# Optimization experiments

Measured on AMD Instinct MI355X. Metric: run time of the kernel, lower is better.

The kernel has to match this reference:

```python
import math
import jax, jax.numpy as jnp
import numpy as np

N = 10000      # num_nodes
E = 320000     # num_edges (avg degree 32)
D = 256        # hidden_dim
H = 8          # num_heads
HD = D // H    # head_dim = 32
S = 3          # num_scales
SCALES = (1.0, 2.0, 4.0)
BASE_MD = 500.0   # max_distance
RADIUS = 50.0     # spatial density radius


def setup_inputs() -> dict:
    key = jax.random.key(0)
    ks = jax.random.split(key, 24)
    nrm = lambda k, shape, s=0.02: jax.random.normal(k, shape, jnp.float32) * s
    return {
        "x": jax.random.normal(ks[0], (N, D), jnp.float32),
        "coords": jax.random.uniform(ks[1], (N, 2), jnp.float32) * 1000.0,
        "edge_index": jax.random.randint(ks[2], (2, E), 0, N, jnp.int32),
        "Wq": nrm(ks[3], (S, D, D)),
        "Wk": nrm(ks[4], (S, D, D)),
        "Wv": nrm(ks[5], (S, D, D)),
        "Wo": nrm(ks[6], (S, D, D)),
        "bo": jnp.zeros((S, D), jnp.float32),
        "temp": jnp.ones((S, H), jnp.float32),
        "dist_emb": nrm(ks[7], (S, 100, HD // 2)),
        "dir_emb": nrm(ks[8], (S, 16, HD // 2)),
        "Wsp1": nrm(ks[9], (S, HD, HD)),
        "bsp1": jnp.zeros((S, HD), jnp.float32),
        "Wsp2": nrm(ks[10], (S, 1, HD)),
        "bsp2": jnp.zeros((S, 1), jnp.float32),
        "Wd1": nrm(ks[11], (S, D // 2, 3)),
        "bd1": jnp.zeros((S, D // 2), jnp.float32),
        "Wd2": nrm(ks[12], (S, D, D // 2)),
        "bd2": jnp.zeros((S, D), jnp.float32),
        "Wf": nrm(ks[13], (D, S * D)),
        "bf": jnp.zeros((D,), jnp.float32),
    }


def reference(x, coords, edge_index, Wq, Wk, Wv, Wo, bo, temp, dist_emb, dir_emb,
              Wsp1, bsp1, Wsp2, bsp2, Wd1, bd1, Wd2, bd2, Wf, bf):
    src, dst = edge_index[0], edge_index[1]   # row=source j, col/dst=target i
    n = x.shape[0]
    eps = 1e-8

    # ---- shared density statistics (same math in every scale's encoder) ----
    ones_e = jnp.ones(src.shape[0], jnp.float32)
    deg = jax.ops.segment_sum(ones_e, src, num_segments=n)
    deg_n = deg / (deg.max() + eps)
    # spatial density: count of neighbors within RADIUS via full cdist (as in torch)
    c = jax.lax.stop_gradient(coords)  # only used via thresholds / integer bins -> zero grad
    d2 = jnp.sqrt(jnp.maximum(((c[:, None, :] - c[None, :, :]) ** 2).sum(-1), 0.0))
    sp = (d2 <= RADIUS).sum(axis=1).astype(jnp.float32) - 1.0
    sp = sp / (sp.max() + eps)
    # local feature variance
    nbr_sum = jax.ops.segment_sum(x[dst], src, num_segments=n)
    cnt = jnp.maximum(deg, 1.0)[:, None]
    fvar = jnp.linalg.norm(x - nbr_sum / cnt, axis=-1)
    fvar = fvar / (fvar.max() + eps)
    dens_raw = jnp.stack([deg_n, sp, fvar], axis=-1)  # [N, 3]

    # ---- shared relative geometry (binned -> no grad through coords) ----
    rel = c[src] - c[dst]                       # coords_j - coords_i
    dist = jnp.linalg.norm(rel, axis=-1)        # [E]
    ang = jnp.arctan2(rel[:, 1], rel[:, 0])
    abin = jnp.clip(((ang + math.pi) / (2.0 * math.pi) * 15.0).astype(jnp.int32), 0, 15)

    outs = []
    for s in range(S):
        md = BASE_MD * SCALES[s]
        dbin = jnp.clip((dist / md * 99.0).astype(jnp.int32), 0, 99)
        se = jnp.concatenate([dist_emb[s][dbin], dir_emb[s][abin]], axis=-1)  # [E, HD]
        enc = (jax.nn.relu(se @ Wsp1[s].T + bsp1[s]) @ Wsp2[s].T + bsp2[s])[:, 0]  # [E]

        df = jax.nn.relu(dens_raw @ Wd1[s].T + bd1[s]) @ Wd2[s].T + bd2[s]  # [N, D]

        q = (x @ Wq[s].T).reshape(n, H, HD)
        k = (x @ Wk[s].T).reshape(n, H, HD)
        v = (x @ Wv[s].T).reshape(n, H, HD)

        scores = (q[dst] * k[src]).sum(-1) / math.sqrt(HD)  # [E, H]
        scores = scores / temp[s][None, :]
        scores = scores + enc[:, None]
        dfi, dfj = df[dst], df[src]
        dsim = (dfi * dfj).sum(-1) / (jnp.maximum(jnp.linalg.norm(dfi, axis=-1), eps)
                                       * jnp.maximum(jnp.linalg.norm(dfj, axis=-1), eps))
        scores = scores * (1.0 + 0.5 * dsim[:, None])

        # scatter-softmax over edges grouped by destination node
        smax = jax.ops.segment_max(scores, dst, num_segments=n)
        p = jnp.exp(scores - smax[dst])
        z = jax.ops.segment_sum(p, dst, num_segments=n)
        probs = p / (z[dst] + 1e-16)

        agg = jax.ops.segment_sum(probs[..., None] * v[src], dst, num_segments=n)
        outs.append(agg.reshape(n, D) @ Wo[s].T + bo[s])

    fused = jnp.concatenate(outs, axis=-1) @ Wf.T + bf
    return fused
```

## Files before the change

### kernel.cpp

```cpp
#include <hip/hip_runtime.h>

typedef _Float16 f16;
typedef _Float16 f16x4 __attribute__((ext_vector_type(4)));
typedef _Float16 f16x8 __attribute__((ext_vector_type(8)));
typedef float    f32x4 __attribute__((ext_vector_type(4)));
typedef float    fv2   __attribute__((ext_vector_type(2)));

__device__ __forceinline__ float4 ld4h(const f16* p) {
  f16x4 t = *(const f16x4*)p;
  return make_float4((float)t[0], (float)t[1], (float)t[2], (float)t[3]);
}

__device__ __forceinline__ float4 dec_fp8x4(unsigned u) {
  fv2 lo = __builtin_amdgcn_cvt_pk_f32_fp8(u, false);
  fv2 hi = __builtin_amdgcn_cvt_pk_f32_fp8(u, true);
  return make_float4(lo[0], lo[1], hi[0], hi[1]);
}

__device__ __forceinline__ unsigned enc_fp8x4(float a, float b, float c, float d) {
  unsigned v = 0;
  v = __builtin_amdgcn_cvt_pk_fp8_f32(a, b, v, false);
  v = __builtin_amdgcn_cvt_pk_fp8_f32(c, d, v, true);
  return v;
}

__device__ __forceinline__ void gld_lds16(const void* g, void* l) {
  __builtin_amdgcn_global_load_lds(
      (const __attribute__((address_space(1))) unsigned*)g,
      (__attribute__((address_space(3))) unsigned*)l, 16, 0, 0);
}

__device__ __forceinline__ int cell_of(const float* coords, int i) {
  int cx = (int)(coords[2 * i] * 0.02f);
  int cy = (int)(coords[2 * i + 1] * 0.02f);
  cx = cx < 0 ? 0 : (cx > 19 ? 19 : cx);
  cy = cy < 0 ? 0 : (cy > 19 ? 19 : cy);
  return cy * 20 + cx;
}

__device__ __forceinline__ void gemm_core(
    f16* As, f16* Bs, int bx, int by, int s,
    const f16* __restrict__ A, int lda, long sA,
    const f16* __restrict__ B, int ldb, long sB,
    const float* __restrict__ bias, int sBias,
    void* __restrict__ Cv, int ldc, long sC, int K, int Mstore, int outMode,
    unsigned char* __restrict__ Cv2, int ldc2, long sC2, int ysplit)
{
  const int tid = threadIdx.x;
  const int lane = tid & 63;
  const int w = tid >> 6;
  const int wr = (w >> 1) * 64, wc = (w & 1) * 64;
  const int srow = tid >> 3;
  const int scol = (((tid & 7) ^ (srow & 7))) * 8;
  const f16* Ab = A + (size_t)s * sA + (size_t)(bx * 128 + srow) * lda + scol;
  const f16* Bb = B + (size_t)s * sB + (size_t)(by * 128 + srow) * ldb + scol;
  char* Asl = (char*)As + tid * 16;
  char* Bsl = (char*)Bs + tid * 16;

  f32x4 acc[4][4] = {};

  for (int kt = 0; kt < K; kt += 64) {
    __syncthreads();
#pragma unroll
    for (int i = 0; i < 4; ++i) {
      gld_lds16(Ab + (size_t)i * 32 * lda + kt, Asl + i * 4096);
      gld_lds16(Bb + (size_t)i * 32 * ldb + kt, Bsl + i * 4096);
    }
    __syncthreads();
#pragma unroll
    for (int kq = 0; kq < 2; ++kq) {
      const int krd = kq * 32 + (lane >> 4) * 8;
      const int kc = krd >> 3;
      f16x8 af[4], bfr[4];
#pragma unroll
      for (int t = 0; t < 4; ++t) {
        const int ra = wr + t * 16 + (lane & 15);
        const int rb = wc + t * 16 + (lane & 15);
        af[t]  = *(const f16x8*)&As[ra * 64 + (kc ^ (ra & 7)) * 8];
        bfr[t] = *(const f16x8*)&Bs[rb * 64 + (kc ^ (rb & 7)) * 8];
      }
#pragma unroll
      for (int mi = 0; mi < 4; ++mi)
#pragma unroll
        for (int ni = 0; ni < 4; ++ni)
          acc[mi][ni] = __builtin_amdgcn_mfma_f32_16x16x32_f16(af[mi], bfr[ni], acc[mi][ni], 0, 0, 0);
    }
  }

  const int r0 = (lane >> 4) << 2;
  const int c0 = lane & 15;
  const bool f8p = (by >= ysplit);
  const int cbase = f8p ? (by - ysplit) * 128 : by * 128;
#pragma unroll
  for (int mi = 0; mi < 4; ++mi) {
#pragma unroll
    for (int ni = 0; ni < 4; ++ni) {
      int col = cbase + wc + ni * 16 + c0;
      float bv = (!f8p && bias) ? bias[s * sBias + col] : 0.0f;
#pragma unroll
      for (int r = 0; r < 4; ++r) {
        int row = bx * 128 + wr + mi * 16 + r0 + r;
        if (row < Mstore) {
          float v = acc[mi][ni][r] + bv;
          if (f8p) {
            unsigned pk = __builtin_amdgcn_cvt_pk_fp8_f32(v, v, 0u, false);
            Cv2[(size_t)s * sC2 + (size_t)row * ldc2 + col] = (unsigned char)(pk & 0xffu);
          } else if (outMode == 1) {
            ((f16*)Cv)[(size_t)s * sC + (size_t)row * ldc + col] = (f16)v;
          } else {
            ((float*)Cv)[(size_t)s * sC + (size_t)row * ldc + col] = v;
          }
        }
      }
    }
  }
}

__global__ __launch_bounds__(256) void prep_kernel(
    const float* __restrict__ x, const float* __restrict__ Wq, const float* __restrict__ Wk,
    const float* __restrict__ Wv, const float* __restrict__ Wd2,
    f16* __restrict__ x_h, unsigned* __restrict__ x8, f16* __restrict__ wqvk,
    f16* __restrict__ wd2h,
    const float* __restrict__ dist_emb, const float* __restrict__ dir_emb,
    const float* __restrict__ Wsp1, const float* __restrict__ bsp1,
    const float* __restrict__ Wsp2, const float* __restrict__ bsp2,
    float* __restrict__ enc_tab,
    const int* __restrict__ eidx, const float* __restrict__ coords,
    int* deg_i, int* indeg_i, int* cellcnt,
    const float* __restrict__ Wf, const float* __restrict__ Wo,
    const float* __restrict__ bo, const float* __restrict__ bf,
    f16* __restrict__ wfo, float* __restrict__ bias_f,
    int E, int N, int hb)
{
  const int b = blockIdx.x;
  if (b < 2048) {
    const int n0 = N * 64;
    const int total = n0 + 147456 + 24576;
    for (int i = b * 256 + threadIdx.x; i < total; i += 2048 * 256) {
      int k = i;
      if (k < n0) {
        float4 v = ((const float4*)x)[k];
        f16x4 o; o[0] = (f16)v.x; o[1] = (f16)v.y; o[2] = (f16)v.z; o[3] = (f16)v.w;
        ((f16x4*)x_h)[k] = o;
        x8[k] = enc_fp8x4(v.x, v.y, v.z, v.w);
        continue;
      }
      const float4* sp; f16x4* dp;
      k -= n0;
      if (k < 147456) {
        int s = k / 49152, r = k % 49152, m = r / 16384, off = r % 16384;
        const float* w = (m == 0) ? Wq : (m == 1) ? Wk : Wv;
        int dblk = (m == 0) ? 0 : (m == 1) ? 32768 : 16384;
        sp = (const float4*)(w + s * 65536) + off;
        dp = (f16x4*)wqvk + s * 49152 + dblk + off;
      } else {
        k -= 147456;
        sp = (const float4*)Wd2 + k; dp = (f16x4*)wd2h + k;
      }
      float4 v = *sp;
      f16x4 o; o[0] = (f16)v.x; o[1] = (f16)v.y; o[2] = (f16)v.z; o[3] = (f16)v.w;
      *dp = o;
    }
  } else if (b < 2067) {
    int id = (b - 2048) * 256 + threadIdx.x;
    if (id >= 3 * 1600) return;
    int s = id / 1600, c = id % 1600, db = c >> 4, ab = c & 15;
    const float* de = dist_emb + (size_t)(s * 100 + db) * 16;
    const float* ae = dir_emb + (size_t)(s * 16 + ab) * 16;
    const float* w1 = Wsp1 + s * 1024;
    const float* b1 = bsp1 + s * 32;
    const float* w2 = Wsp2 + s * 32;
    float enc = bsp2[s];
    for (int j = 0; j < 32; ++j) {
      float a = b1[j];
      const float* wr = w1 + j * 32;
#pragma unroll
      for (int i = 0; i < 16; ++i) a += de[i] * wr[i];
#pragma unroll
      for (int i = 0; i < 16; ++i) a += ae[i] * wr[16 + i];
      enc += fmaxf(a, 0.0f) * w2[j];
    }
    enc_tab[id] = enc;
  } else if (b < 2067 + hb) {
    int e = (b - 2067) * 256 + threadIdx.x;
    if (e < E) {
      atomicAdd(&deg_i[eidx[e]], 1);
      atomicAdd(&indeg_i[eidx[E + e]], 1);
    }
    if (e < N) atomicAdd(&cellcnt[cell_of(coords, e)], 1);
  } else if (b < 2067 + hb + 96) {
    __shared__ float wf8[8][256];
    int idx = b - (2067 + hb);
    int s = idx / 32;
    int og = (idx % 32) * 8;
    int j = threadIdx.x;
#pragma unroll
    for (int oo = 0; oo < 8; ++oo) wf8[oo][j] = Wf[(og + oo) * 768 + s * 256 + j];
    __syncthreads();
    const float* wo = Wo + (size_t)s * 65536 + j;
    float acc[8] = {0.f, 0.f, 0.f, 0.f, 0.f, 0.f, 0.f, 0.f};
    for (int m = 0; m < 256; ++m) {
      float val = wo[(size_t)m * 256];
#pragma unroll
      for (int oo = 0; oo < 8; ++oo) acc[oo] = fmaf(wf8[oo][m], val, acc[oo]);
    }
#pragma unroll
    for (int oo = 0; oo < 8; ++oo)
      wfo[(size_t)(og + oo) * 768 + s * 256 + j] = (f16)acc[oo];
  } else {
    int j = threadIdx.x;
    float acc = bf[j];
    const float* wr = Wf + (size_t)j * 768;
    for (int t = 0; t < 768; ++t) acc = fmaf(bo[t], wr[t], acc);
    bias_f[j] = acc;
  }
}

__global__ __launch_bounds__(1024) void scan_kernel(const int* __restrict__ indeg,
                                                    const int* __restrict__ deg,
                                                    const int* __restrict__ cellcnt,
                                                    int* dptr, int* sptr, int* cptr,
                                                    int* __restrict__ perm, int N)
{
  __shared__ int lds[1024];
  __shared__ int cnt[256], scn2[256], fill[256];
  const int tid = threadIdx.x;
  const int pass = blockIdx.x;
  if (pass == 3) {
    if (tid < 256) { cnt[tid] = 0; fill[tid] = 0; }
    __syncthreads();
    for (int n = tid; n < N; n += 1024) {
      int d = indeg[n];
      int key = 255 - (d > 255 ? 255 : d);
      atomicAdd(&cnt[key], 1);
    }
    __syncthreads();
    if (tid < 256) scn2[tid] = cnt[tid];
    __syncthreads();
    for (int off = 1; off < 256; off <<= 1) {
      int v = 0;
      if (tid < 256 && tid >= off) v = scn2[tid - off];
      __syncthreads();
      if (tid < 256) scn2[tid] += v;
      __syncthreads();
    }
    for (int n = tid; n < N; n += 1024) {
      int d = indeg[n];
      int key = 255 - (d > 255 ? 255 : d);
      int pos = scn2[key] - cnt[key] + atomicAdd(&fill[key], 1);
      perm[pos] = n;
    }
    return;
  }
  const int* in = (pass == 0) ? indeg : (pass == 1) ? deg : cellcnt;
  int* out = (pass == 0) ? dptr : (pass == 1) ? sptr : cptr;
  int len = (pass == 2) ? 400 : N;
  int base = tid * 16;
  int loc[16];
  int sum = 0;
#pragma unroll
  for (int j = 0; j < 16; ++j) {
    int v = (base + j < len) ? in[base + j] : 0;
    loc[j] = sum; sum += v;
  }
  lds[tid] = sum;
  __syncthreads();
  for (int off = 1; off < 1024; off <<= 1) {
    int t = (tid >= off) ? lds[tid - off] : 0;
    __syncthreads();
    lds[tid] += t;
    __syncthreads();
  }
  int prev = tid ? lds[tid - 1] : 0;
#pragma unroll
  for (int j = 0; j < 16; ++j)
    if (base + j < len) out[base + j] = prev + loc[j];
  if (tid == 1023) out[len] = lds[1023];
}

__global__ __launch_bounds__(256) void scatter_kernel(
    const int* __restrict__ eidx, const float* __restrict__ coords,
    const int* __restrict__ dptr, const int* __restrict__ sptr, const int* __restrict__ cptr,
    int* fill_d, int* fill_s, int* fill_c,
    int2* __restrict__ erec, int* __restrict__ sdst, float2* __restrict__ scoord, int E, int N)
{
  int e = blockIdx.x * 256 + threadIdx.x;
  if (e < E) {
    int s = eidx[e], d = eidx[E + e];
    float rx = coords[2 * s] - coords[2 * d];
    float ry = coords[2 * s + 1] - coords[2 * d + 1];
    float dist = sqrtf(rx * rx + ry * ry);
    float ang = atan2f(ry, rx);
    int ab = (int)((ang + 3.14159265358979323846f) / 6.28318530717958647692f * 15.0f);
    ab = ab < 0 ? 0 : (ab > 15 ? 15 : ab);
    int b0 = (int)((dist / 500.0f) * 99.0f);  b0 = b0 < 0 ? 0 : (b0 > 99 ? 99 : b0);
    int b1 = (int)((dist / 1000.0f) * 99.0f); b1 = b1 < 0 ? 0 : (b1 > 99 ? 99 : b1);
    int b2 = (int)((dist / 2000.0f) * 99.0f); b2 = b2 < 0 ? 0 : (b2 > 99 ? 99 : b2);
    unsigned pb = (unsigned)b0 | ((unsigned)b1 << 7) | ((unsigned)b2 << 14) | ((unsigned)ab << 21);
    int pd = dptr[d] + atomicAdd(&fill_d[d], 1);
    erec[pd] = make_int2(s, (int)pb);
    int ps = sptr[s] + atomicAdd(&fill_s[s], 1);
    sdst[ps] = d;
  }
  if (e < N) {
    int cid = cell_of(coords, e);
    int pc = cptr[cid] + atomicAdd(&fill_c[cid], 1);
    scoord[pc] = ((const float2*)coords)[e];
  }
}

__global__ __launch_bounds__(256) void mid_kernel(
    const f16* __restrict__ x_h, const f16* __restrict__ wqvk,
    f16* __restrict__ nrec3, unsigned char* __restrict__ krec3,
    const float* __restrict__ coords, const float2* __restrict__ scoord,
    const int* __restrict__ cptr,
    const float* __restrict__ x, const unsigned* __restrict__ x8,
    const int* __restrict__ sptr, const int* __restrict__ sdst,
    int* __restrict__ sp_i, float* __restrict__ fvar,
    int N, int Mp, int mtiles, int qkvB)
{
  __shared__ f16 As[128 * 64];
  __shared__ f16 Bs[128 * 64];
  const int b = blockIdx.x;
  if (b < qkvB) {
    int bx = b % mtiles;
    int t = b / mtiles;
    gemm_core(As, Bs, bx, t % 6, t / 6,
              x_h, 256, 0, wqvk, 256, 196608, nullptr, 0,
              nrec3, 512, (long)Mp * 512, 256, Mp, 1,
              krec3, 256, (long)Mp * 256, 4);
    return;
  }
  int wv = threadIdx.x >> 6, lane = threadIdx.x & 63;
  int node = (b - qkvB) * 4 + wv;
  if (node >= N) return;

  float cx = coords[2 * node], cy = coords[2 * node + 1];
  {
    int gx = (int)(cx * 0.02f); gx = gx < 0 ? 0 : (gx > 19 ? 19 : gx);
    int gy = (int)(cy * 0.02f); gy = gy < 0 ? 0 : (gy > 19 ? 19 : gy);
    int x0 = gx > 0 ? gx - 1 : 0, x1 = gx < 19 ? gx + 1 : 19;
    int y0 = gy > 0 ? gy - 1 : 0, y1 = gy < 19 ? gy + 1 : 19;
    int cnt = 0;
    for (int r = y0; r <= y1; ++r) {
      int j0 = cptr[r * 20 + x0], j1 = cptr[r * 20 + x1 + 1];
      for (int j = j0 + lane; j < j1; j += 64) {
        float2 c = scoord[j];
        float dx = cx - c.x, dy = cy - c.y;
        cnt += (dx * dx + dy * dy <= 2500.0f) ? 1 : 0;
      }
    }
    cnt += __shfl_xor(cnt, 1);  cnt += __shfl_xor(cnt, 2);  cnt += __shfl_xor(cnt, 4);
    cnt += __shfl_xor(cnt, 8);  cnt += __shfl_xor(cnt, 16); cnt += __shfl_xor(cnt, 32);
    if (lane == 0) sp_i[node] = cnt;
  }

  const int slot = lane >> 3, w = lane & 7;
  float sum[32];
#pragma unroll
  for (int i = 0; i < 32; ++i) sum[i] = 0.f;
  int e0 = sptr[node], e1 = sptr[node + 1];
  int nit = (e1 - e0 + 7) >> 3;
  for (int it = 0; it < nit; ++it) {
    int e = e0 + it * 8 + slot;
    bool valid = e < e1;
    int dd = sdst[valid ? e : e1 - 1];
    const unsigned* xp = x8 + dd * 64 + w * 8;
    uint4 a = *(const uint4*)xp;
    uint4 bq = *(const uint4*)(xp + 4);
    float vm = valid ? 1.f : 0.f;
    unsigned wd[8] = {a.x, a.y, a.z, a.w, bq.x, bq.y, bq.z, bq.w};
#pragma unroll
    for (int k = 0; k < 8; ++k) {
      float4 f = dec_fp8x4(wd[k]);
      sum[k*4+0] = fmaf(vm, f.x, sum[k*4+0]);
      sum[k*4+1] = fmaf(vm, f.y, sum[k*4+1]);
      sum[k*4+2] = fmaf(vm, f.z, sum[k*4+2]);
      sum[k*4+3] = fmaf(vm, f.w, sum[k*4+3]);
    }
  }
#pragma unroll
  for (int i = 0; i < 32; ++i) {
    sum[i] += __shfl_xor(sum[i], 8);
    sum[i] += __shfl_xor(sum[i], 16);
    sum[i] += __shfl_xor(sum[i], 32);
  }
  float rcnt = 1.0f / fmaxf((float)(e1 - e0), 1.0f);
  const float4* xp4 = (const float4*)(x + (size_t)node * 256 + w * 32);
  float ss = 0.f;
#pragma unroll
  for (int k = 0; k < 8; ++k) {
    float4 xm = xp4[k];
    float d0 = xm.x - sum[k*4+0] * rcnt;
    float d1 = xm.y - sum[k*4+1] * rcnt;
    float d2 = xm.z - sum[k*4+2] * rcnt;
    float d3 = xm.w - sum[k*4+3] * rcnt;
    ss += d0*d0 + d1*d1 + d2*d2 + d3*d3;
  }
  ss += __shfl_xor(ss, 1);  ss += __shfl_xor(ss, 2);  ss += __shfl_xor(ss, 4);
  ss += __shfl_xor(ss, 8);  ss += __shfl_xor(ss, 16); ss += __shfl_xor(ss, 32);
  if (lane == 0) fvar[node] = sqrtf(ss * 0.125f);
}

__global__ __launch_bounds__(1024) void maxred_kernel(
    const int* __restrict__ sptr, const int* __restrict__ sp_i,
    const float* __restrict__ fvar, float* __restrict__ maxf, int N)
{
  __shared__ float l0[1024], l1[1024], l2[1024];
  int tid = threadIdx.x;
  float m0 = 0.f, m1 = 0.f, m2 = 0.f;
  for (int i = tid; i < N; i += 1024) {
    m0 = fmaxf(m0, (float)(sptr[i + 1] - sptr[i]));
    m1 = fmaxf(m1, (float)(sp_i[i] - 1));
    m2 = fmaxf(m2, fvar[i]);
  }
  l0[tid] = m0; l1[tid] = m1; l2[tid] = m2;
  __syncthreads();
  for (int off = 512; off > 0; off >>= 1) {
    if (tid < off) {
      l0[tid] = fmaxf(l0[tid], l0[tid + off]);
      l1[tid] = fmaxf(l1[tid], l1[tid + off]);
      l2[tid] = fmaxf(l2[tid], l2[tid + off]);
    }
    __syncthreads();
  }
  if (tid == 0) { maxf[0] = l0[0]; maxf[1] = l1[0]; maxf[2] = l2[0]; }
}

__global__ __launch_bounds__(256) void gemm_wd2(
    const int* __restrict__ sptr, const int* __restrict__ sp_i, const float* __restrict__ fvar,
    const float* __restrict__ maxf, const float* __restrict__ Wd1, const float* __restrict__ bd1,
    const f16* __restrict__ B, const float* __restrict__ bd2,
    f16* __restrict__ dfh, int N, int Mp)
{
  __shared__ f16 As[128 * 64];
  __shared__ f16 Bs[128 * 64];
  const int s = blockIdx.z;
  const int tid = threadIdx.x;
  const int lane = tid & 63;
  const int w = tid >> 6;
  const int wr = (w >> 1) * 64, wc = (w & 1) * 64;
  const int srow = tid >> 3;
  const int c = tid & 7;
  const int scolB = ((c ^ (srow & 7))) * 8;
  const f16* Bb = B + (size_t)s * 32768 + (size_t)(blockIdx.y * 128 + srow) * 128 + scolB;
  char* Bsl = (char*)Bs + tid * 16;
  const float dm = maxf[0] + 1e-8f, sm = maxf[1] + 1e-8f, fm = maxf[2] + 1e-8f;

  f32x4 acc[4][4] = {};

  for (int kt = 0; kt < 128; kt += 64) {
    __syncthreads();
#pragma unroll
    for (int i = 0; i < 4; ++i)
      gld_lds16(Bb + (size_t)i * 32 * 128 + kt, Bsl + i * 4096);
#pragma unroll
    for (int i = 0; i < 4; ++i) {
      int r = srow + i * 32;
      int node = blockIdx.x * 128 + r;
      float d0 = 0.f, d1 = 0.f, d2 = 0.f;
      if (node < N) {
        d0 = (float)(sptr[node + 1] - sptr[node]) / dm;
        d1 = (float)(sp_i[node] - 1) / sm;
        d2 = fvar[node] / fm;
      }
      int kc8 = c ^ (r & 7);
      const float* w1 = Wd1 + s * 384 + (kt + kc8 * 8) * 3;
      const float* b1 = bd1 + s * 128 + kt + kc8 * 8;
      f16x8 hv;
#pragma unroll
      for (int j = 0; j < 8; ++j) {
        float h = fmaf(w1[j*3], d0, fmaf(w1[j*3+1], d1, fmaf(w1[j*3+2], d2, b1[j])));
        hv[j] = (f16)fmaxf(h, 0.f);
      }
      *(f16x8*)&As[r * 64 + c * 8] = hv;
    }
    __syncthreads();
#pragma unroll
    for (int kq = 0; kq < 2; ++kq) {
      const int krd = kq * 32 + (lane >> 4) * 8;
      const int kc = krd >> 3;
      f16x8 af[4], bfr[4];
#pragma unroll
      for (int t = 0; t < 4; ++t) {
        const int ra = wr + t * 16 + (lane & 15);
        const int rb = wc + t * 16 + (lane & 15);
        af[t]  = *(const f16x8*)&As[ra * 64 + (kc ^ (ra & 7)) * 8];
        bfr[t] = *(const f16x8*)&Bs[rb * 64 + (kc ^ (rb & 7)) * 8];
      }
#pragma unroll
      for (int mi = 0; mi < 4; ++mi)
#pragma unroll
        for (int ni = 0; ni < 4; ++ni)
          acc[mi][ni] = __builtin_amdgcn_mfma_f32_16x16x32_f16(af[mi], bfr[ni], acc[mi][ni], 0, 0, 0);
    }
  }

  const int r0 = (lane >> 4) << 2;
  const int c0 = lane & 15;
#pragma unroll
  for (int mi = 0; mi < 4; ++mi) {
#pragma unroll
    for (int ni = 0; ni < 4; ++ni) {
      int col = blockIdx.y * 128 + wc + ni * 16 + c0;
      float bv = bd2[s * 256 + col];
#pragma unroll
      for (int r = 0; r < 4; ++r) {
        int row = blockIdx.x * 128 + wr + mi * 16 + r0 + r;
        dfh[(size_t)s * Mp * 256 + (size_t)row * 256 + col] = (f16)(acc[mi][ni][r] + bv);
      }
    }
  }
}

__global__ __launch_bounds__(256) void gemm_bt_f16(
    const f16* __restrict__ A, int lda, long sA,
    const f16* __restrict__ B, int ldb, long sB,
    const float* __restrict__ bias, int sBias,
    void* __restrict__ Cv, int ldc, long sC, int K, int Mstore, int outMode,
    unsigned char* __restrict__ Cv2, int ldc2, long sC2, int ysplit)
{
  __shared__ f16 As[128 * 64];
  __shared__ f16 Bs[128 * 64];
  gemm_core(As, Bs, blockIdx.x, blockIdx.y, blockIdx.z,
            A, lda, sA, B, ldb, sB, bias, sBias,
            Cv, ldc, sC, K, Mstore, outMode, Cv2, ldc2, sC2, ysplit);
}

__global__ __launch_bounds__(256) void norm_kernel(const f16* __restrict__ dfh,
                                                   unsigned* __restrict__ drec8, int N, int Mp)
{
  int wv = threadIdx.x >> 6, lane = threadIdx.x & 63;
  int node = blockIdx.x * 4 + wv;
  if (node >= N) return;
  int s = blockIdx.y;
  float4 d = ld4h(dfh + (size_t)s * Mp * 256 + (size_t)node * 256 + lane * 4);
  float ss = d.x * d.x + d.y * d.y + d.z * d.z + d.w * d.w;
  ss += __shfl_xor(ss, 1);  ss += __shfl_xor(ss, 2);  ss += __shfl_xor(ss, 4);
  ss += __shfl_xor(ss, 8);  ss += __shfl_xor(ss, 16); ss += __shfl_xor(ss, 32);
  float rn = 1.0f / fmaxf(sqrtf(ss), 1e-8f);
  drec8[(size_t)s * Mp * 64 + node * 64 + lane] = enc_fp8x4(d.x * rn, d.y * rn, d.z * rn, d.w * rn);
}

__global__ __launch_bounds__(256) void edge_attn(
    const f16* __restrict__ nrec0, const unsigned* __restrict__ krec0,
    const unsigned* __restrict__ drec0, const int2* __restrict__ erec,
    const int* __restrict__ dptr, const int* __restrict__ perm,
    const float* __restrict__ enc_tab, const float* __restrict__ temp,
    f16* __restrict__ aggc, int N, int Mp)
{
  int wv = threadIdx.x >> 6, lane = threadIdx.x & 63;
  int node = blockIdx.x * 4 + wv;
  if (node >= N) return;
  node = perm[node];
  const int s = blockIdx.y;
  const int sshift = 7 * s;
  const f16* nrec = nrec0 + (size_t)s * Mp * 512;
  const unsigned* krec8 = krec0 + (size_t)s * Mp * 64;
  const unsigned* drec8 = drec0 + (size_t)s * Mp * 64;
  const float* enc_s = enc_tab + s * 1600;

  const int slot = lane >> 4;
  const int sub  = lane & 15;
  const int hd   = sub >> 1;
  const int half = sub & 1;
  const int doff = hd * 8 + half * 4;
  const int voff = hd * 32 + half * 16;

  float qf[16];
  {
    const f16* qp = nrec + (size_t)node * 512 + voff;
    f16x8 a = *(const f16x8*)qp;
    f16x8 b = *(const f16x8*)(qp + 8);
#pragma unroll
    for (int j = 0; j < 8; ++j) { qf[j] = (float)a[j]; qf[8 + j] = (float)b[j]; }
  }
  uint4 diw = *(const uint4*)(drec8 + node * 64 + doff);
  const float inv_th = 0.17677669529663687f / temp[s * 8 + hd];

  float m = -1e30f, z = 0.f;
  float acc[16];
#pragma unroll
  for (int i = 0; i < 16; ++i) acc[i] = 0.f;

  int e0 = dptr[node], e1 = dptr[node + 1];
  int nit = (e1 - e0 + 3) >> 2;
  if (nit > 0) {
    int ce = e0 + slot; if (ce >= e1) ce = e1 - 1;
    int2 recA = erec[ce];
    for (int it = 0; it < nit; ++it) {
      int en = e0 + (it + 1) * 4 + slot; en = (en < e1) ? en : e1 - 1;
      int2 recN = erec[en];

      int e = e0 + it * 4 + slot;
      bool valid = e < e1;
      int src = recA.x;
      unsigned pb = (unsigned)recA.y;
      uint4 kwv = *(const uint4*)(krec8 + src * 64 + doff);
      uint4 dwv = *(const uint4*)(drec8 + src * 64 + doff);
      const f16* vp = nrec + (size_t)src * 512 + 256 + voff;
      f16x8 vs0 = *(const f16x8*)vp;
      f16x8 vs1 = *(const f16x8*)(vp + 8);
      float enc = enc_s[((pb >> sshift) & 127u) * 16 + (pb >> 21)];

      unsigned kw[4] = {kwv.x, kwv.y, kwv.z, kwv.w};
      unsigned dw[4] = {dwv.x, dwv.y, dwv.z, dwv.w};
      unsigned di[4] = {diw.x, diw.y, diw.z, diw.w};
      float qk0 = 0.f, qk1 = 0.f, ds0 = 0.f, ds1 = 0.f;
#pragma unroll
      for (int w = 0; w < 4; ++w) {
        float4 kf = dec_fp8x4(kw[w]);
        qk0 = fmaf(qf[w*4+0], kf.x, qk0);
        qk1 = fmaf(qf[w*4+1], kf.y, qk1);
        qk0 = fmaf(qf[w*4+2], kf.z, qk0);
        qk1 = fmaf(qf[w*4+3], kf.w, qk1);
        float4 df = dec_fp8x4(dw[w]);
        float4 dd = dec_fp8x4(di[w]);
        ds0 = fmaf(dd.x, df.x, ds0);
        ds1 = fmaf(dd.y, df.y, ds1);
        ds0 = fmaf(dd.z, df.z, ds0);
        ds1 = fmaf(dd.w, df.w, ds1);
      }
      float qk = qk0 + qk1;
      float ds = ds0 + ds1;
      qk += __shfl_xor(qk, 1);
      ds += __shfl_xor(ds, 1); ds += __shfl_xor(ds, 2);
      ds += __shfl_xor(ds, 4); ds += __shfl_xor(ds, 8);

      float sc = (qk * inv_th + enc) * (1.0f + 0.5f * ds);
      sc = valid ? sc : -1e30f;
      if (__any(sc > m + 8.0f)) {
        float mn = fmaxf(m, sc);
        float rs = __expf(m - mn);
        z *= rs;
#pragma unroll
        for (int i = 0; i < 16; ++i) acc[i] *= rs;
        m = mn;
      }
      float p = __expf(sc - m) * (valid ? 1.0f : 0.0f);
      z += p;
#pragma unroll
      for (int j = 0; j < 8; ++j) acc[j]     = fmaf(p, (float)vs0[j], acc[j]);
#pragma unroll
      for (int j = 0; j < 8; ++j) acc[8 + j] = fmaf(p, (float)vs1[j], acc[8 + j]);

      recA = recN;
    }
  }

  float M = m;
  M = fmaxf(M, __shfl_xor(M, 16));
  M = fmaxf(M, __shfl_xor(M, 32));
  float f = __expf(m - M);
  z *= f;
  z += __shfl_xor(z, 16); z += __shfl_xor(z, 32);
#pragma unroll
  for (int i = 0; i < 16; ++i) {
    float a = acc[i] * f;
    a += __shfl_xor(a, 16); a += __shfl_xor(a, 32);
    acc[i] = a;
  }
  float rz = 1.0f / (z + 1e-16f);
  if (slot == 0) {
    f16* op = aggc + (size_t)node * 768 + s * 256 + voff;
    f16x8 o0, o1;
#pragma unroll
    for (int j = 0; j < 8; ++j) { o0[j] = (f16)(acc[j] * rz); o1[j] = (f16)(acc[8 + j] * rz); }
    *(f16x8*)op = o0;
    *(f16x8*)(op + 8) = o1;
  }
}

extern "C" void kernel_launch(void* const* d_in, const int* in_sizes, int n_in,
                              void* d_out, int out_size, void* d_ws, size_t ws_size,
                              hipStream_t stream)
{
  const float* x      = (const float*)d_in[0];
  const float* coords = (const float*)d_in[1];
  const int*   eidx   = (const int*)  d_in[2];
  const float* Wq   = (const float*)d_in[3];
  const float* Wk   = (const float*)d_in[4];
  const float* Wv   = (const float*)d_in[5];
  const float* Wo   = (const float*)d_in[6];
  const float* bo   = (const float*)d_in[7];
  const float* temp = (const float*)d_in[8];
  const float* dist_emb = (const float*)d_in[9];
  const float* dir_emb  = (const float*)d_in[10];
  const float* Wsp1 = (const float*)d_in[11];
  const float* bsp1 = (const float*)d_in[12];
  const float* Wsp2 = (const float*)d_in[13];
  const float* bsp2 = (const float*)d_in[14];
  const float* Wd1  = (const float*)d_in[15];
  const float* bd1  = (const float*)d_in[16];
  const float* Wd2  = (const float*)d_in[17];
  const float* bd2  = (const float*)d_in[18];
  const float* Wf   = (const float*)d_in[19];
  const float* bf   = (const float*)d_in[20];
  (void)n_in; (void)out_size; (void)ws_size;

  const int N  = in_sizes[0] / 256;
  const int E  = in_sizes[2] / 2;
  const int Mp = ((N + 127) / 128) * 128;

  char* p = (char*)d_ws;
  auto alloc = [&](size_t b) -> void* {
    void* r = (void*)p;
    p += (b + 255) & ~(size_t)255;
    return r;
  };

  f16*      x_h   = (f16*)     alloc((size_t)Mp * 256 * 2);
  unsigned* x8    = (unsigned*)alloc((size_t)Mp * 256);
  f16*      nrec3 = (f16*)     alloc((size_t)3 * Mp * 512 * 2);
  unsigned* krec3 = (unsigned*)alloc((size_t)3 * Mp * 256);
  unsigned* drec3 = (unsigned*)alloc((size_t)3 * Mp * 256);
  f16*      dfh3  = (f16*)     alloc((size_t)3 * Mp * 256 * 2);
  f16*      aggc  = (f16*)     alloc((size_t)Mp * 768 * 2);
  f16*      wqvk  = (f16*)     alloc((size_t)3 * 768 * 256 * 2);
  f16*      wfo   = (f16*)     alloc((size_t)256 * 768 * 2);
  float*    bias_f = (float*)  alloc(256 * 4);
  f16*      wd2h  = (f16*)     alloc((size_t)3 * 256 * 128 * 2);
  float*    enc_tab = (float*) alloc((size_t)3 * 1600 * 4);
  int*    dptr = (int*)   alloc((size_t)(N + 1) * 4);
  int*    sptr = (int*)   alloc((size_t)(N + 1) * 4);
  int*    cptr = (int*)   alloc((size_t)401 * 4);
  int*    perm = (int*)   alloc((size_t)N * 4);
  int2*   erec = (int2*)  alloc((size_t)E * 8);
  int*    sdst = (int*)   alloc((size_t)E * 4);
  float2* scoord = (float2*)alloc((size_t)N * 8);
  float*  fvar = (float*) alloc((size_t)N * 4);
  int*    sp_i = (int*)   alloc((size_t)N * 4);
  float*  maxf = (float*) alloc(4 * 4);
  char* z0 = p;
  int* deg_i   = (int*)alloc((size_t)N * 4);
  int* indeg_i = (int*)alloc((size_t)N * 4);
  int* fill_d  = (int*)alloc((size_t)N * 4);
  int* fill_s  = (int*)alloc((size_t)N * 4);
  int* cellcnt = (int*)alloc(400 * 4);
  int* fill_c  = (int*)alloc(400 * 4);
  size_t zbytes = (size_t)(p - z0);
  hipMemsetAsync(z0, 0, zbytes, stream);

  const int hb = (E + 255) / 256;
  prep_kernel<<<2067 + hb + 96 + 1, 256, 0, stream>>>(
      x, Wq, Wk, Wv, Wd2, x_h, x8, wqvk, wd2h,
      dist_emb, dir_emb, Wsp1, bsp1, Wsp2, bsp2, enc_tab,
      eidx, coords, deg_i, indeg_i, cellcnt,
      Wf, Wo, bo, bf, wfo, bias_f, E, N, hb);
  scan_kernel<<<4, 1024, 0, stream>>>(indeg_i, deg_i, cellcnt, dptr, sptr, cptr, perm, N);
  scatter_kernel<<<(E + 255) / 256, 256, 0, stream>>>(eidx, coords, dptr, sptr, cptr,
                                                      fill_d, fill_s, fill_c, erec, sdst, scoord, E, N);
  const int mtiles = Mp / 128;
  const int qkvB = mtiles * 18;
  mid_kernel<<<qkvB + (N + 3) / 4, 256, 0, stream>>>(
      x_h, wqvk, nrec3, (unsigned char*)krec3,
      coords, scoord, cptr, x, x8, sptr, sdst, sp_i, fvar,
      N, Mp, mtiles, qkvB);
  maxred_kernel<<<1, 1024, 0, stream>>>(sptr, sp_i, fvar, maxf, N);
  gemm_wd2<<<dim3(mtiles, 2, 3), 256, 0, stream>>>(sptr, sp_i, fvar, maxf, Wd1, bd1,
                                                   wd2h, bd2, dfh3, N, Mp);
  norm_kernel<<<dim3((N + 3) / 4, 3), 256, 0, stream>>>(dfh3, drec3, N, Mp);
  edge_attn<<<dim3((N + 3) / 4, 3), 256, 0, stream>>>(nrec3, krec3, drec3, erec, dptr, perm,
                                                      enc_tab, temp, aggc, N, Mp);
  gemm_bt_f16<<<dim3(mtiles, 2, 1), 256, 0, stream>>>(aggc, 768, 0,
                                                      wfo, 768, 0, bias_f, 0,
                                                      d_out, 256, 0, 768, N, 0,
                                                      nullptr, 0, 0, 99);
}
```

Before: 332.2 us.

## Fuse row L2 normalization and fp8 encoding into the Wd2 density GEMM

```diff
diff --git a/kernel.cpp b/kernel.cpp
--- a/kernel.cpp
+++ b/kernel.cpp
@@ -427,33 +427,37 @@
   if (tid == 0) { maxf[0] = l0[0]; maxf[1] = l1[0]; maxf[2] = l2[0]; }
 }
 
-__global__ __launch_bounds__(256) void gemm_wd2(
+__global__ __launch_bounds__(256) void gemm_wd2norm(
     const int* __restrict__ sptr, const int* __restrict__ sp_i, const float* __restrict__ fvar,
     const float* __restrict__ maxf, const float* __restrict__ Wd1, const float* __restrict__ bd1,
     const f16* __restrict__ B, const float* __restrict__ bd2,
-    f16* __restrict__ dfh, int N, int Mp)
-{
-  __shared__ f16 As[128 * 64];
-  __shared__ f16 Bs[128 * 64];
+    unsigned* __restrict__ drec8, int N, int Mp)
+{
+  __shared__ char ldsbuf[49152];
+  __shared__ float ssrow[2][128];
+  f16* As = (f16*)ldsbuf;
+  f16* Bs = (f16*)(ldsbuf + 16384);
   const int s = blockIdx.z;
   const int tid = threadIdx.x;
   const int lane = tid & 63;
   const int w = tid >> 6;
-  const int wr = (w >> 1) * 64, wc = (w & 1) * 64;
+  const int wr = (w >> 1) * 64;
+  const int wc = (w & 1) * 128;
   const int srow = tid >> 3;
   const int c = tid & 7;
-  const int scolB = ((c ^ (srow & 7))) * 8;
-  const f16* Bb = B + (size_t)s * 32768 + (size_t)(blockIdx.y * 128 + srow) * 128 + scolB;
   char* Bsl = (char*)Bs + tid * 16;
   const float dm = maxf[0] + 1e-8f, sm = maxf[1] + 1e-8f, fm = maxf[2] + 1e-8f;
-
-  f32x4 acc[4][4] = {};
+  const int scolB = (c ^ (srow & 7)) * 8;
+
+  f32x4 acc[4][8] = {};
 
   for (int kt = 0; kt < 128; kt += 64) {
     __syncthreads();
 #pragma unroll
-    for (int i = 0; i < 4; ++i)
-      gld_lds16(Bb + (size_t)i * 32 * 128 + kt, Bsl + i * 4096);
+    for (int i = 0; i < 8; ++i) {
+      int rB = srow + i * 32;
+      gld_lds16(B + (size_t)s * 32768 + (size_t)rB * 128 + scolB + kt, Bsl + i * 4096);
+    }
 #pragma unroll
     for (int i = 0; i < 4; ++i) {
       int r = srow + i * 32;
@@ -480,36 +484,80 @@
     for (int kq = 0; kq < 2; ++kq) {
       const int krd = kq * 32 + (lane >> 4) * 8;
       const int kc = krd >> 3;
-      f16x8 af[4], bfr[4];
+      f16x8 af[4], bfr[8];
 #pragma unroll
       for (int t = 0; t < 4; ++t) {
         const int ra = wr + t * 16 + (lane & 15);
-        const int rb = wc + t * 16 + (lane & 15);
-        af[t]  = *(const f16x8*)&As[ra * 64 + (kc ^ (ra & 7)) * 8];
-        bfr[t] = *(const f16x8*)&Bs[rb * 64 + (kc ^ (rb & 7)) * 8];
+        af[t] = *(const f16x8*)&As[ra * 64 + (kc ^ (ra & 7)) * 8];
+      }
+#pragma unroll
+      for (int ni = 0; ni < 8; ++ni) {
+        const int rb = wc + ni * 16 + (lane & 15);
+        bfr[ni] = *(const f16x8*)&Bs[rb * 64 + (kc ^ (rb & 7)) * 8];
       }
 #pragma unroll
       for (int mi = 0; mi < 4; ++mi)
 #pragma unroll
-        for (int ni = 0; ni < 4; ++ni)
+        for (int ni = 0; ni < 8; ++ni)
           acc[mi][ni] = __builtin_amdgcn_mfma_f32_16x16x32_f16(af[mi], bfr[ni], acc[mi][ni], 0, 0, 0);
     }
   }
 
   const int r0 = (lane >> 4) << 2;
   const int c0 = lane & 15;
+  float bv[8];
+#pragma unroll
+  for (int ni = 0; ni < 8; ++ni) bv[ni] = bd2[s * 256 + wc + ni * 16 + c0];
 #pragma unroll
   for (int mi = 0; mi < 4; ++mi) {
 #pragma unroll
-    for (int ni = 0; ni < 4; ++ni) {
-      int col = blockIdx.y * 128 + wc + ni * 16 + c0;
-      float bv = bd2[s * 256 + col];
-#pragma unroll
-      for (int r = 0; r < 4; ++r) {
-        int row = blockIdx.x * 128 + wr + mi * 16 + r0 + r;
-        dfh[(size_t)s * Mp * 256 + (size_t)row * 256 + col] = (f16)(acc[mi][ni][r] + bv);
-      }
-    }
+    for (int rr = 0; rr < 4; ++rr) {
+      float ssl = 0.f;
+#pragma unroll
+      for (int ni = 0; ni < 8; ++ni) {
+        float v = acc[mi][ni][rr] + bv[ni];
+        acc[mi][ni][rr] = v;
+        ssl = fmaf(v, v, ssl);
+      }
+      ssl += __shfl_xor(ssl, 1); ssl += __shfl_xor(ssl, 2);
+      ssl += __shfl_xor(ssl, 4); ssl += __shfl_xor(ssl, 8);
+      if (c0 == 0) ssrow[w & 1][wr + mi * 16 + r0 + rr] = ssl;
+    }
+  }
+  __syncthreads();
+
+  f16* S = (f16*)ldsbuf;
+  for (int half = 0; half < 2; ++half) {
+    if ((w >> 1) == half) {
+#pragma unroll
+      for (int mi = 0; mi < 4; ++mi) {
+#pragma unroll
+        for (int rr = 0; rr < 4; ++rr) {
+          int R = wr + mi * 16 + r0 + rr;
+          float rn = 1.0f / fmaxf(sqrtf(ssrow[0][R] + ssrow[1][R]), 1e-8f);
+          int rl = R - half * 64;
+#pragma unroll
+          for (int ni = 0; ni < 8; ++ni)
+            S[rl * 264 + wc + ni * 16 + c0] = (f16)(acc[mi][ni][rr] * rn);
+        }
+      }
+    }
+    __syncthreads();
+    {
+      int rl = tid >> 2;
+      int seg = tid & 3;
+      int node = blockIdx.x * 128 + half * 64 + rl;
+      const f16* src = S + rl * 264 + seg * 64;
+      unsigned ow[16];
+#pragma unroll
+      for (int t = 0; t < 16; ++t)
+        ow[t] = enc_fp8x4((float)src[t*4], (float)src[t*4+1], (float)src[t*4+2], (float)src[t*4+3]);
+      unsigned* dst = drec8 + (size_t)s * Mp * 64 + (size_t)node * 64 + seg * 16;
+#pragma unroll
+      for (int t = 0; t < 4; ++t)
+        *(uint4*)(dst + t * 4) = make_uint4(ow[t*4], ow[t*4+1], ow[t*4+2], ow[t*4+3]);
+    }
+    __syncthreads();
   }
 }
 
@@ -525,21 +573,6 @@
   gemm_core(As, Bs, blockIdx.x, blockIdx.y, blockIdx.z,
             A, lda, sA, B, ldb, sB, bias, sBias,
             Cv, ldc, sC, K, Mstore, outMode, Cv2, ldc2, sC2, ysplit);
-}
-
-__global__ __launch_bounds__(256) void norm_kernel(const f16* __restrict__ dfh,
-                                                   unsigned* __restrict__ drec8, int N, int Mp)
-{
-  int wv = threadIdx.x >> 6, lane = threadIdx.x & 63;
-  int node = blockIdx.x * 4 + wv;
-  if (node >= N) return;
-  int s = blockIdx.y;
-  float4 d = ld4h(dfh + (size_t)s * Mp * 256 + (size_t)node * 256 + lane * 4);
-  float ss = d.x * d.x + d.y * d.y + d.z * d.z + d.w * d.w;
-  ss += __shfl_xor(ss, 1);  ss += __shfl_xor(ss, 2);  ss += __shfl_xor(ss, 4);
-  ss += __shfl_xor(ss, 8);  ss += __shfl_xor(ss, 16); ss += __shfl_xor(ss, 32);
-  float rn = 1.0f / fmaxf(sqrtf(ss), 1e-8f);
-  drec8[(size_t)s * Mp * 64 + node * 64 + lane] = enc_fp8x4(d.x * rn, d.y * rn, d.z * rn, d.w * rn);
 }
 
 __global__ __launch_bounds__(256) void edge_attn(
@@ -603,6 +636,7 @@
       f16x8 vs1 = *(const f16x8*)(vp + 8);
       float enc = enc_s[((pb >> sshift) & 127u) * 16 + (pb >> 21)];
 
+      __builtin_amdgcn_s_setprio(1);
       unsigned kw[4] = {kwv.x, kwv.y, kwv.z, kwv.w};
       unsigned dw[4] = {dwv.x, dwv.y, dwv.z, dwv.w};
       unsigned di[4] = {diw.x, diw.y, diw.z, diw.w};
@@ -643,6 +677,7 @@
       for (int j = 0; j < 8; ++j) acc[j]     = fmaf(p, (float)vs0[j], acc[j]);
 #pragma unroll
       for (int j = 0; j < 8; ++j) acc[8 + j] = fmaf(p, (float)vs1[j], acc[8 + j]);
+      __builtin_amdgcn_s_setprio(0);
 
       recA = recN;
     }
@@ -714,7 +749,6 @@
   f16*      nrec3 = (f16*)     alloc((size_t)3 * Mp * 512 * 2);
   unsigned* krec3 = (unsigned*)alloc((size_t)3 * Mp * 256);
   unsigned* drec3 = (unsigned*)alloc((size_t)3 * Mp * 256);
-  f16*      dfh3  = (f16*)     alloc((size_t)3 * Mp * 256 * 2);
   f16*      aggc  = (f16*)     alloc((size_t)Mp * 768 * 2);
   f16*      wqvk  = (f16*)     alloc((size_t)3 * 768 * 256 * 2);
   f16*      wfo   = (f16*)     alloc((size_t)256 * 768 * 2);
@@ -757,9 +791,8 @@
       coords, scoord, cptr, x, x8, sptr, sdst, sp_i, fvar,
       N, Mp, mtiles, qkvB);
   maxred_kernel<<<1, 1024, 0, stream>>>(sptr, sp_i, fvar, maxf, N);
-  gemm_wd2<<<dim3(mtiles, 2, 3), 256, 0, stream>>>(sptr, sp_i, fvar, maxf, Wd1, bd1,
-                                                   wd2h, bd2, dfh3, N, Mp);
-  norm_kernel<<<dim3((N + 3) / 4, 3), 256, 0, stream>>>(dfh3, drec3, N, Mp);
+  gemm_wd2norm<<<dim3(mtiles, 1, 3), 256, 0, stream>>>(sptr, sp_i, fvar, maxf, Wd1, bd1,
+                                                       wd2h, bd2, drec3, N, Mp);
   edge_attn<<<dim3((N + 3) / 4, 3), 256, 0, stream>>>(nrec3, krec3, drec3, erec, dptr, perm,
                                                       enc_tab, temp, aggc, N, Mp);
   gemm_bt_f16<<<dim3(mtiles, 2, 1), 256, 0, stream>>>(aggc, 768, 0,
```

Measured after the change: 336.0 us. Within noise of the previous version (+1.2%).
